# Kernel tuning notes

Measured on AMD Instinct MI355X. Metric: run time of the kernel, lower is better.

## Reference

```python
import jax, jax.numpy as jnp
import numpy as np
import math

B, S, HID = 2, 2048, 1024
NH = 16
HD = HID // NH


def setup_inputs() -> dict:
    key = jax.random.key(0)
    ks = jax.random.split(key, 5)
    std = 1.0 / math.sqrt(HID)
    return {
        "x": jax.random.normal(ks[0], (B, S, HID), dtype=jnp.float32),
        "wq": jax.random.normal(ks[1], (HID, HID), dtype=jnp.float32) * std,
        "wk": jax.random.normal(ks[2], (HID, HID), dtype=jnp.float32) * std,
        "wv": jax.random.normal(ks[3], (HID, HID), dtype=jnp.float32) * std,
        "wo": jax.random.normal(ks[4], (HID, HID), dtype=jnp.float32) * std,
    }


def reference(x, wq, wk, wv, wo):
    # x: [B, S, HID]; weights stored as nn.Linear weight [out, in] -> y = x @ W.T
    b, s, _ = x.shape
    scale = 1.0 / math.sqrt(HD)

    def heads(t):  # [B, S, HID] -> [B, NH, S, HD]
        return t.reshape(b, s, NH, HD).transpose(0, 2, 1, 3)

    q = heads(x @ wq.T)
    k = heads(x @ wk.T)
    v = heads(x @ wv.T)

    # single ring step (cp_size=1): streaming-LSE causal attention
    scores = jnp.einsum("bhqd,bhkd->bhqk", q, k) * scale  # [B, NH, S, S]
    q_idx = jnp.arange(s)[:, None]
    k_idx = jnp.arange(s)[None, :]
    causal_mask = k_idx > q_idx  # [S, S]
    scores = jnp.where(causal_mask, -jnp.inf, scores)

    local_max = jnp.max(scores, axis=-1, keepdims=True)
    exp_scores = jnp.exp(scores - local_max)
    local_sum = jnp.sum(exp_scores, axis=-1, keepdims=True)
    attn_num = jnp.einsum("bhqk,bhkd->bhqd", exp_scores, v)
    attn_out = attn_num / (local_sum + 1e-8)  # [B, NH, S, HD]

    attn_out = attn_out.transpose(0, 2, 1, 3).reshape(b, s, HID)
    return attn_out @ wo.T
```

## Files before the change

### kernel.cpp

```cpp
#include <hip/hip_runtime.h>
#include <hip/hip_bf16.h>

#define S_LEN 2048
#define NHEAD 16
#define HDIM 64
#define HID 1024
#define BATCH 2
#define TSTR 136

typedef __attribute__((ext_vector_type(8))) short s16x8;
typedef __attribute__((ext_vector_type(4))) short s16x4;
typedef __attribute__((ext_vector_type(4))) float f32x4;

__device__ __forceinline__ short f2bf(float f) {
    union { __hip_bfloat16 b; short s; } u;
    u.b = __float2bfloat16(f);
    return u.s;
}
__device__ __forceinline__ float fexp2(float x) {
    return __builtin_amdgcn_exp2f(x);
}
__device__ __forceinline__ f32x4 mfma16(s16x8 a, s16x8 b, f32x4 c) {
    return __builtin_amdgcn_mfma_f32_16x16x32_bf16(a, b, c, 0, 0, 0);
}
__device__ __forceinline__ void gload16(const short* g, short* l) {
    __builtin_amdgcn_global_load_lds(
        (const __attribute__((address_space(1))) void*)g,
        (__attribute__((address_space(3))) void*)l, 16, 0, 0);
}
__device__ __forceinline__ unsigned bfpack(float a, float b) {
    unsigned ua = __builtin_bit_cast(unsigned, a) + 0x8000u;
    unsigned ub = __builtin_bit_cast(unsigned, b) + 0x8000u;
    return (ub & 0xFFFF0000u) | (ua >> 16);
}

__global__ __launch_bounds__(256) void convert_kernel(
    const float* __restrict__ x,  const float* __restrict__ wq,
    const float* __restrict__ wk, const float* __restrict__ wv,
    const float* __restrict__ wo,
    short* __restrict__ xb, short* __restrict__ wcat, short* __restrict__ wob)
{
    const int F4X = 1048576, F4W = 262144;
    const int total = F4X + 4 * F4W;
    for (int i = blockIdx.x * blockDim.x + threadIdx.x; i < total;
         i += gridDim.x * blockDim.x) {
        const float4* s; short* d; int off;
        if (i < F4X)              { s = (const float4*)x;  d = xb;             off = i; }
        else if (i < F4X + F4W)   { s = (const float4*)wq; d = wcat;           off = i - F4X; }
        else if (i < F4X + 2*F4W) { s = (const float4*)wk; d = wcat + 1048576; off = i - (F4X + F4W); }
        else if (i < F4X + 3*F4W) { s = (const float4*)wv; d = wcat + 2097152; off = i - (F4X + 2*F4W); }
        else                      { s = (const float4*)wo; d = wob;            off = i - (F4X + 3*F4W); }
        float4 v = s[off];
        s16x4 o4 = { f2bf(v.x), f2bf(v.y), f2bf(v.z), f2bf(v.w) };
        *(s16x4*)(d + (size_t)off * 4) = o4;
    }
}

__global__ __launch_bounds__(256) void qkv_gemm2(
    const short* __restrict__ xb, const short* __restrict__ wcat,
    short* __restrict__ q_ws, short* __restrict__ k_ws, short* __restrict__ vt_ws)
{
    __shared__ union SM {
        struct { short A[128][64]; short B[128][64]; } s;
        short T[128][TSTR];
    } sm;
    const int t = threadIdx.x;
    const int lane = t & 63, w = t >> 6;
    const int g = lane >> 4, r15 = lane & 15;
    const int wm = w >> 1, wn = w & 1;
    const int bid = blockIdx.x;
    const int cx = bid & 7, ii = bid >> 3;
    const int mt = cx * 4 + (ii & 3), nt = ii >> 2;
    const int m0 = mt * 128, n0 = nt * 128;
    const int sel = n0 >> 10;
    const int nr0 = n0 & 1023;
    const short* Ag = (sel == 2) ? (wcat + (size_t)(2048 + nr0) * 1024)
                                 : (xb   + (size_t)m0 * 1024);
    const short* Bg = (sel == 2) ? (xb   + (size_t)m0 * 1024)
                                 : (wcat + (size_t)(sel * 1024 + nr0) * 1024);
    const int lrow = lane >> 3;
    const int scol = ((lane & 7) ^ lrow) * 8;
    const int rsw = r15 & 7;
    const float osc = (sel == 0) ? 0.125f : ((sel == 1) ? 1.44269504f : 1.0f);

    f32x4 acc[4][4] = {};

    for (int k0 = 0; k0 < 1024; k0 += 64) {
        __syncthreads();
        #pragma unroll
        for (int ch = 0; ch < 4; ++ch) {
            const int row = w * 32 + ch * 8;
            gload16(Ag + (size_t)(row + lrow) * 1024 + k0 + scol, &sm.s.A[row][0]);
            gload16(Bg + (size_t)(row + lrow) * 1024 + k0 + scol, &sm.s.B[row][0]);
        }
        __syncthreads();
        #pragma unroll
        for (int kk = 0; kk < 2; ++kk) {
            s16x8 af[4], bfr[4];
            #pragma unroll
            for (int mi = 0; mi < 4; ++mi)
                af[mi] = *(const s16x8*)&sm.s.A[wm * 64 + mi * 16 + r15][((kk * 4 + g) ^ rsw) * 8];
            #pragma unroll
            for (int ni = 0; ni < 4; ++ni)
                bfr[ni] = *(const s16x8*)&sm.s.B[wn * 64 + ni * 16 + r15][((kk * 4 + g) ^ rsw) * 8];
            #pragma unroll
            for (int mi = 0; mi < 4; ++mi)
                #pragma unroll
                for (int ni = 0; ni < 4; ++ni)
                    acc[mi][ni] = mfma16(af[mi], bfr[ni], acc[mi][ni]);
        }
    }

    __syncthreads();
    #pragma unroll
    for (int mi = 0; mi < 4; ++mi)
    #pragma unroll
    for (int ni = 0; ni < 4; ++ni)
        #pragma unroll
        for (int reg = 0; reg < 4; ++reg)
            sm.T[wm * 64 + mi * 16 + g * 4 + reg][wn * 64 + ni * 16 + r15]
                = f2bf(acc[mi][ni][reg] * osc);
    __syncthreads();

    const int b = m0 >> 11;
    const int ms = m0 & 2047;
    #pragma unroll
    for (int it = 0; it < 8; ++it) {
        int u = w + it * 4;
        int half = u & 1;
        int rg = u >> 1;
        int r = rg * 8 + lrow;
        int colc = half * 64 + (lane & 7) * 8;
        s16x8 v = *(const s16x8*)&sm.T[r][colc];
        if (sel == 2) {
            int n = nr0 + r;
            int h = n >> 6, d = n & 63;
            *(s16x8*)(vt_ws + ((size_t)(b * NHEAD + h) * HDIM + d) * S_LEN + ms + colc) = v;
        } else {
            int s = ms + r;
            int n = nr0 + colc;
            int h = n >> 6, d = n & 63;
            short* dst = (sel == 0) ? q_ws : k_ws;
            *(s16x8*)(dst + ((size_t)(b * NHEAD + h) * S_LEN + s) * HDIM + d) = v;
        }
    }
}

__global__ __launch_bounds__(128) void attn_kernel6(
    const short* __restrict__ q_ws, const short* __restrict__ k_ws,
    const short* __restrict__ vt_ws, short* __restrict__ attn_ws)
{
    __shared__ short Ks[2][64][64];
    __shared__ short Vts[2][64][64];
    const int t = threadIdx.x;
    const int lane = t & 63, w = t >> 6;
    const int g = lane >> 4, r15 = lane & 15;
    const int bid = blockIdx.x;
    const int lb = (bid & 7) * 128 + (bid >> 3);
    const int pi = lb & 31;
    const int bh = lb >> 5;
    const size_t base = (size_t)bh * S_LEN * HDIM;
    const int swr = (r15 & 7) << 3;
    const int b = bh >> 4, h = bh & 15;

    const int r0 = t >> 3, c0 = (t & 7) * 8;
    const int cx0 = c0 ^ ((r0 & 7) << 3);

    union P8 { unsigned u[4]; s16x8 v; };
    union V8 { s16x4 h[2]; s16x8 v; };

    for (int phase = 0; phase < 2; ++phase) {
        const int qt32 = phase ? (63 - pi) : pi;
        const int q0 = qt32 * 32;
        const int ntk = (qt32 >> 1) + 1;
        const int qg = q0 + w * 16 + r15;
        const int qrel = qg - (ntk - 1) * 64;
        s16x8 qf0 = *(const s16x8*)(q_ws + base + (size_t)qg * HDIM + g * 8);
        s16x8 qf1 = *(const s16x8*)(q_ws + base + (size_t)qg * HDIM + 32 + g * 8);
        f32x4 o[4] = {};
        float lrun_p = 0.f;

        #pragma unroll
        for (int j = 0; j < 4; ++j) {
            int r = r0 + j * 16;
            *(s16x8*)&Ks[0][r][cx0]  = *(const s16x8*)(k_ws  + base + (size_t)r * HDIM + c0);
            *(s16x8*)&Vts[0][r][cx0] = *(const s16x8*)(vt_ws + base + (size_t)r * S_LEN + c0);
        }
        __syncthreads();

        const short* kp = k_ws  + base + (size_t)(64 + r0) * HDIM + c0;
        const short* vp = vt_ws + base + (size_t)r0 * S_LEN + 64 + c0;

        for (int kt = 0; kt < ntk; ++kt) {
            const int cur = kt & 1;
            const bool pre = (kt + 1 < ntk);
            const bool dg = (kt == ntk - 1);
            s16x8 ka[4], va[4];
            if (pre) {
                #pragma unroll
                for (int j = 0; j < 4; ++j) {
                    ka[j] = *(const s16x8*)(kp + (size_t)j * 16 * HDIM);
                    va[j] = *(const s16x8*)(vp + (size_t)j * 16 * S_LEN);
                }
                kp += (size_t)64 * HDIM; vp += 64;
            }

            s16x8 kfa[4][2];
            #pragma unroll
            for (int f = 0; f < 4; ++f)
                #pragma unroll
                for (int c = 0; c < 2; ++c)
                    kfa[f][c] = *(const s16x8*)&Ks[cur][f * 16 + r15][(c * 32 + g * 8) ^ swr];
            V8 vfr[4][2];
            #pragma unroll
            for (int f2 = 0; f2 < 4; ++f2)
                #pragma unroll
                for (int kc = 0; kc < 2; ++kc) {
                    vfr[f2][kc].h[0] = *(const s16x4*)&Vts[cur][f2 * 16 + r15][(kc * 32 + g * 4) ^ swr];
                    vfr[f2][kc].h[1] = *(const s16x4*)&Vts[cur][f2 * 16 + r15][(kc * 32 + 16 + g * 4) ^ swr];
                }

            f32x4 z[4];
            __builtin_amdgcn_s_setprio(1);
            #pragma unroll
            for (int f = 0; f < 4; ++f) {
                f32x4 zz = { 0.f, 0.f, 0.f, 0.f };
                zz = mfma16(kfa[f][0], qf0, zz);
                zz = mfma16(kfa[f][1], qf1, zz);
                z[f] = zz;
            }
            __builtin_amdgcn_s_setprio(0);

            if (dg) {
                #pragma unroll
                for (int f = 0; f < 4; ++f)
                    #pragma unroll
                    for (int reg = 0; reg < 4; ++reg)
                        if (f * 16 + g * 4 + reg > qrel) z[f][reg] = -3e30f;
            }

            P8 p8[2];
            #pragma unroll
            for (int f = 0; f < 4; ++f) {
                float e0 = fexp2(z[f][0]);
                float e1 = fexp2(z[f][1]);
                float e2 = fexp2(z[f][2]);
                float e3 = fexp2(z[f][3]);
                lrun_p += (e0 + e1) + (e2 + e3);
                p8[f >> 1].u[(f & 1) * 2]     = bfpack(e0, e1);
                p8[f >> 1].u[(f & 1) * 2 + 1] = bfpack(e2, e3);
            }

            __builtin_amdgcn_s_setprio(1);
            #pragma unroll
            for (int f2 = 0; f2 < 4; ++f2) {
                o[f2] = mfma16(vfr[f2][0].v, p8[0].v, o[f2]);
                o[f2] = mfma16(vfr[f2][1].v, p8[1].v, o[f2]);
            }
            __builtin_amdgcn_s_setprio(0);

            if (pre) {
                #pragma unroll
                for (int j = 0; j < 4; ++j) {
                    int r = r0 + j * 16;
                    *(s16x8*)&Ks[cur ^ 1][r][cx0]  = ka[j];
                    *(s16x8*)&Vts[cur ^ 1][r][cx0] = va[j];
                }
            }
            __syncthreads();
        }

        float lr = lrun_p;
        lr += __shfl_xor(lr, 16);
        lr += __shfl_xor(lr, 32);
        float inv = 1.f / (lr + 1e-8f);
        size_t obase = ((size_t)b * S_LEN + qg) * HID + h * HDIM + g * 4;
        #pragma unroll
        for (int f2 = 0; f2 < 4; ++f2) {
            s16x4 ov = { f2bf(o[f2][0] * inv), f2bf(o[f2][1] * inv),
                         f2bf(o[f2][2] * inv), f2bf(o[f2][3] * inv) };
            *(s16x4*)(attn_ws + obase + f2 * 16) = ov;
        }
        __syncthreads();
    }
}

__global__ __launch_bounds__(256) void wo_gemm2(
    const short* __restrict__ attn, const short* __restrict__ wob,
    float* __restrict__ out)
{
    __shared__ short As[128][64];
    __shared__ short Bs[128][64];
    const int t = threadIdx.x;
    const int lane = t & 63, w = t >> 6;
    const int g = lane >> 4, r15 = lane & 15;
    const int wm = w >> 1, wn = w & 1;
    const int bid = blockIdx.x;
    const int cx = bid & 7, ii = bid >> 3;
    const int mt = cx * 4 + (ii & 3), nt = ii >> 2;
    const int m0 = mt * 128, n0 = nt * 128;
    const int lrow = lane >> 3;
    const int scol = ((lane & 7) ^ lrow) * 8;
    const int rsw = r15 & 7;

    f32x4 acc[4][4] = {};

    for (int k0 = 0; k0 < 1024; k0 += 64) {
        __syncthreads();
        #pragma unroll
        for (int ch = 0; ch < 4; ++ch) {
            const int row = w * 32 + ch * 8;
            gload16(attn + (size_t)(m0 + row + lrow) * 1024 + k0 + scol, &As[row][0]);
            gload16(wob  + (size_t)(n0 + row + lrow) * 1024 + k0 + scol, &Bs[row][0]);
        }
        __syncthreads();
        #pragma unroll
        for (int kk = 0; kk < 2; ++kk) {
            s16x8 af[4], bfr[4];
            #pragma unroll
            for (int mi = 0; mi < 4; ++mi)
                af[mi] = *(const s16x8*)&As[wm * 64 + mi * 16 + r15][((kk * 4 + g) ^ rsw) * 8];
            #pragma unroll
            for (int ni = 0; ni < 4; ++ni)
                bfr[ni] = *(const s16x8*)&Bs[wn * 64 + ni * 16 + r15][((kk * 4 + g) ^ rsw) * 8];
            #pragma unroll
            for (int mi = 0; mi < 4; ++mi)
                #pragma unroll
                for (int ni = 0; ni < 4; ++ni)
                    acc[mi][ni] = mfma16(af[mi], bfr[ni], acc[mi][ni]);
        }
    }

    #pragma unroll
    for (int mi = 0; mi < 4; ++mi)
    #pragma unroll
    for (int ni = 0; ni < 4; ++ni) {
        #pragma unroll
        for (int reg = 0; reg < 4; ++reg) {
            int m = m0 + wm * 64 + mi * 16 + g * 4 + reg;
            int n = n0 + wn * 64 + ni * 16 + r15;
            out[(size_t)m * 1024 + n] = acc[mi][ni][reg];
        }
    }
}

extern "C" void kernel_launch(void* const* d_in, const int* in_sizes, int n_in,
                              void* d_out, int out_size, void* d_ws, size_t ws_size,
                              hipStream_t stream) {
    const float* x  = (const float*)d_in[0];
    const float* wq = (const float*)d_in[1];
    const float* wk = (const float*)d_in[2];
    const float* wv = (const float*)d_in[3];
    const float* wo = (const float*)d_in[4];
    float* out = (float*)d_out;

    const size_t ELEMS = (size_t)BATCH * S_LEN * HID;
    short* q_ws    = (short*)d_ws;
    short* k_ws    = q_ws + ELEMS;
    short* vt_ws   = k_ws + ELEMS;
    short* xb      = vt_ws + ELEMS;
    short* attn_ws = xb;
    short* wcat    = xb + ELEMS;
    short* wob     = wcat + 3145728;

    convert_kernel<<<dim3(2048), dim3(256), 0, stream>>>(x, wq, wk, wv, wo, xb, wcat, wob);
    qkv_gemm2<<<dim3(768), dim3(256), 0, stream>>>(xb, wcat, q_ws, k_ws, vt_ws);
    attn_kernel6<<<dim3(1024), dim3(128), 0, stream>>>(q_ws, k_ws, vt_ws, attn_ws);
    wo_gemm2<<<dim3(256), dim3(256), 0, stream>>>(attn_ws, wob, out);
}
```

Baseline: 117.6 us.

## Process paired causal query tiles in one pass sharing K/V loads

```diff
diff --git a/kernel.cpp b/kernel.cpp
--- a/kernel.cpp
+++ b/kernel.cpp
@@ -146,7 +146,7 @@
     }
 }
 
-__global__ __launch_bounds__(128) void attn_kernel6(
+__global__ __launch_bounds__(128) void attn_kernel8(
     const short* __restrict__ q_ws, const short* __restrict__ k_ws,
     const short* __restrict__ vt_ws, short* __restrict__ attn_ws)
 {
@@ -156,9 +156,10 @@
     const int lane = t & 63, w = t >> 6;
     const int g = lane >> 4, r15 = lane & 15;
     const int bid = blockIdx.x;
-    const int lb = (bid & 7) * 128 + (bid >> 3);
-    const int pi = lb & 31;
-    const int bh = lb >> 5;
+    const int cx = bid & 7, ii = bid >> 3;
+    const int bh = cx * 4 + (ii >> 5);
+    const int v5 = ii & 31;
+    const int pi = (v5 & 1) ? (31 - (v5 >> 1)) : (v5 >> 1);
     const size_t base = (size_t)bh * S_LEN * HDIM;
     const int swr = (r15 & 7) << 3;
     const int b = bh >> 4, h = bh & 15;
@@ -169,76 +170,79 @@
     union P8 { unsigned u[4]; s16x8 v; };
     union V8 { s16x4 h[2]; s16x8 v; };
 
-    for (int phase = 0; phase < 2; ++phase) {
-        const int qt32 = phase ? (63 - pi) : pi;
-        const int q0 = qt32 * 32;
-        const int ntk = (qt32 >> 1) + 1;
-        const int qg = q0 + w * 16 + r15;
-        const int qrel = qg - (ntk - 1) * 64;
-        s16x8 qf0 = *(const s16x8*)(q_ws + base + (size_t)qg * HDIM + g * 8);
-        s16x8 qf1 = *(const s16x8*)(q_ws + base + (size_t)qg * HDIM + 32 + g * 8);
-        f32x4 o[4] = {};
-        float lrun_p = 0.f;
-
-        #pragma unroll
-        for (int j = 0; j < 4; ++j) {
-            int r = r0 + j * 16;
-            *(s16x8*)&Ks[0][r][cx0]  = *(const s16x8*)(k_ws  + base + (size_t)r * HDIM + c0);
-            *(s16x8*)&Vts[0][r][cx0] = *(const s16x8*)(vt_ws + base + (size_t)r * S_LEN + c0);
-        }
-        __syncthreads();
-
-        const short* kp = k_ws  + base + (size_t)(64 + r0) * HDIM + c0;
-        const short* vp = vt_ws + base + (size_t)r0 * S_LEN + 64 + c0;
-
-        for (int kt = 0; kt < ntk; ++kt) {
-            const int cur = kt & 1;
-            const bool pre = (kt + 1 < ntk);
-            const bool dg = (kt == ntk - 1);
-            s16x8 ka[4], va[4];
-            if (pre) {
-                #pragma unroll
-                for (int j = 0; j < 4; ++j) {
-                    ka[j] = *(const s16x8*)(kp + (size_t)j * 16 * HDIM);
-                    va[j] = *(const s16x8*)(vp + (size_t)j * 16 * S_LEN);
-                }
-                kp += (size_t)64 * HDIM; vp += 64;
-            }
-
-            s16x8 kfa[4][2];
-            #pragma unroll
-            for (int f = 0; f < 4; ++f)
-                #pragma unroll
-                for (int c = 0; c < 2; ++c)
-                    kfa[f][c] = *(const s16x8*)&Ks[cur][f * 16 + r15][(c * 32 + g * 8) ^ swr];
-            V8 vfr[4][2];
-            #pragma unroll
-            for (int f2 = 0; f2 < 4; ++f2)
-                #pragma unroll
-                for (int kc = 0; kc < 2; ++kc) {
-                    vfr[f2][kc].h[0] = *(const s16x4*)&Vts[cur][f2 * 16 + r15][(kc * 32 + g * 4) ^ swr];
-                    vfr[f2][kc].h[1] = *(const s16x4*)&Vts[cur][f2 * 16 + r15][(kc * 32 + 16 + g * 4) ^ swr];
-                }
-
+    const int qtA = pi, qtB = 63 - pi;
+    const int ntkA = (qtA >> 1) + 1;
+    const int ntkB = (qtB >> 1) + 1;
+    const int qgA = qtA * 32 + w * 16 + r15;
+    const int qgB = qtB * 32 + w * 16 + r15;
+    const int qrelA = qgA - (ntkA - 1) * 64;
+    const int qrelB = qgB - (ntkB - 1) * 64;
+
+    s16x8 qfA0 = *(const s16x8*)(q_ws + base + (size_t)qgA * HDIM + g * 8);
+    s16x8 qfA1 = *(const s16x8*)(q_ws + base + (size_t)qgA * HDIM + 32 + g * 8);
+    s16x8 qfB0 = *(const s16x8*)(q_ws + base + (size_t)qgB * HDIM + g * 8);
+    s16x8 qfB1 = *(const s16x8*)(q_ws + base + (size_t)qgB * HDIM + 32 + g * 8);
+    f32x4 oA[4] = {}, oB[4] = {};
+    float lrA = 0.f, lrB = 0.f;
+
+    #pragma unroll
+    for (int j = 0; j < 4; ++j) {
+        int r = r0 + j * 16;
+        *(s16x8*)&Ks[0][r][cx0]  = *(const s16x8*)(k_ws  + base + (size_t)r * HDIM + c0);
+        *(s16x8*)&Vts[0][r][cx0] = *(const s16x8*)(vt_ws + base + (size_t)r * S_LEN + c0);
+    }
+    __syncthreads();
+
+    const short* kp = k_ws  + base + (size_t)(64 + r0) * HDIM + c0;
+    const short* vp = vt_ws + base + (size_t)r0 * S_LEN + 64 + c0;
+
+    for (int kt = 0; kt < ntkB; ++kt) {
+        const int cur = kt & 1;
+        const bool pre = (kt + 1 < ntkB);
+        s16x8 ka[4], va[4];
+        if (pre) {
+            #pragma unroll
+            for (int j = 0; j < 4; ++j) {
+                ka[j] = *(const s16x8*)(kp + (size_t)j * 16 * HDIM);
+                va[j] = *(const s16x8*)(vp + (size_t)j * 16 * S_LEN);
+            }
+            kp += (size_t)64 * HDIM; vp += 64;
+        }
+
+        s16x8 kfa[4][2];
+        #pragma unroll
+        for (int f = 0; f < 4; ++f)
+            #pragma unroll
+            for (int c = 0; c < 2; ++c)
+                kfa[f][c] = *(const s16x8*)&Ks[cur][f * 16 + r15][(c * 32 + g * 8) ^ swr];
+        V8 vfr[4][2];
+        #pragma unroll
+        for (int f2 = 0; f2 < 4; ++f2)
+            #pragma unroll
+            for (int kc = 0; kc < 2; ++kc) {
+                vfr[f2][kc].h[0] = *(const s16x4*)&Vts[cur][f2 * 16 + r15][(kc * 32 + g * 4) ^ swr];
+                vfr[f2][kc].h[1] = *(const s16x4*)&Vts[cur][f2 * 16 + r15][(kc * 32 + 16 + g * 4) ^ swr];
+            }
+
+        {
+            const bool dg = (kt == ntkB - 1);
             f32x4 z[4];
             __builtin_amdgcn_s_setprio(1);
             #pragma unroll
             for (int f = 0; f < 4; ++f) {
                 f32x4 zz = { 0.f, 0.f, 0.f, 0.f };
-                zz = mfma16(kfa[f][0], qf0, zz);
-                zz = mfma16(kfa[f][1], qf1, zz);
+                zz = mfma16(kfa[f][0], qfB0, zz);
+                zz = mfma16(kfa[f][1], qfB1, zz);
                 z[f] = zz;
             }
             __builtin_amdgcn_s_setprio(0);
-
             if (dg) {
                 #pragma unroll
                 for (int f = 0; f < 4; ++f)
                     #pragma unroll
                     for (int reg = 0; reg < 4; ++reg)
-                        if (f * 16 + g * 4 + reg > qrel) z[f][reg] = -3e30f;
-            }
-
+                        if (f * 16 + g * 4 + reg > qrelB) z[f][reg] = -3e30f;
+            }
             P8 p8[2];
             #pragma unroll
             for (int f = 0; f < 4; ++f) {
@@ -246,42 +250,94 @@
                 float e1 = fexp2(z[f][1]);
                 float e2 = fexp2(z[f][2]);
                 float e3 = fexp2(z[f][3]);
-                lrun_p += (e0 + e1) + (e2 + e3);
+                lrB += (e0 + e1) + (e2 + e3);
                 p8[f >> 1].u[(f & 1) * 2]     = bfpack(e0, e1);
                 p8[f >> 1].u[(f & 1) * 2 + 1] = bfpack(e2, e3);
             }
-
             __builtin_amdgcn_s_setprio(1);
             #pragma unroll
             for (int f2 = 0; f2 < 4; ++f2) {
-                o[f2] = mfma16(vfr[f2][0].v, p8[0].v, o[f2]);
-                o[f2] = mfma16(vfr[f2][1].v, p8[1].v, o[f2]);
+                oB[f2] = mfma16(vfr[f2][0].v, p8[0].v, oB[f2]);
+                oB[f2] = mfma16(vfr[f2][1].v, p8[1].v, oB[f2]);
             }
             __builtin_amdgcn_s_setprio(0);
-
-            if (pre) {
+        }
+
+        if (kt < ntkA) {
+            const bool dg = (kt == ntkA - 1);
+            f32x4 z[4];
+            __builtin_amdgcn_s_setprio(1);
+            #pragma unroll
+            for (int f = 0; f < 4; ++f) {
+                f32x4 zz = { 0.f, 0.f, 0.f, 0.f };
+                zz = mfma16(kfa[f][0], qfA0, zz);
+                zz = mfma16(kfa[f][1], qfA1, zz);
+                z[f] = zz;
+            }
+            __builtin_amdgcn_s_setprio(0);
+            if (dg) {
                 #pragma unroll
-                for (int j = 0; j < 4; ++j) {
-                    int r = r0 + j * 16;
-                    *(s16x8*)&Ks[cur ^ 1][r][cx0]  = ka[j];
-                    *(s16x8*)&Vts[cur ^ 1][r][cx0] = va[j];
-                }
-            }
-            __syncthreads();
-        }
-
-        float lr = lrun_p;
-        lr += __shfl_xor(lr, 16);
-        lr += __shfl_xor(lr, 32);
-        float inv = 1.f / (lr + 1e-8f);
-        size_t obase = ((size_t)b * S_LEN + qg) * HID + h * HDIM + g * 4;
+                for (int f = 0; f < 4; ++f)
+                    #pragma unroll
+                    for (int reg = 0; reg < 4; ++reg)
+                        if (f * 16 + g * 4 + reg > qrelA) z[f][reg] = -3e30f;
+            }
+            P8 p8[2];
+            #pragma unroll
+            for (int f = 0; f < 4; ++f) {
+                float e0 = fexp2(z[f][0]);
+                float e1 = fexp2(z[f][1]);
+                float e2 = fexp2(z[f][2]);
+                float e3 = fexp2(z[f][3]);
+                lrA += (e0 + e1) + (e2 + e3);
+                p8[f >> 1].u[(f & 1) * 2]     = bfpack(e0, e1);
+                p8[f >> 1].u[(f & 1) * 2 + 1] = bfpack(e2, e3);
+            }
+            __builtin_amdgcn_s_setprio(1);
+            #pragma unroll
+            for (int f2 = 0; f2 < 4; ++f2) {
+                oA[f2] = mfma16(vfr[f2][0].v, p8[0].v, oA[f2]);
+                oA[f2] = mfma16(vfr[f2][1].v, p8[1].v, oA[f2]);
+            }
+            __builtin_amdgcn_s_setprio(0);
+        }
+
+        if (pre) {
+            #pragma unroll
+            for (int j = 0; j < 4; ++j) {
+                int r = r0 + j * 16;
+                *(s16x8*)&Ks[cur ^ 1][r][cx0]  = ka[j];
+                *(s16x8*)&Vts[cur ^ 1][r][cx0] = va[j];
+            }
+        }
+        __syncthreads();
+    }
+
+    {
+        float l = lrA;
+        l += __shfl_xor(l, 16);
+        l += __shfl_xor(l, 32);
+        float inv = 1.f / (l + 1e-8f);
+        size_t obase = ((size_t)b * S_LEN + qgA) * HID + h * HDIM + g * 4;
         #pragma unroll
         for (int f2 = 0; f2 < 4; ++f2) {
-            s16x4 ov = { f2bf(o[f2][0] * inv), f2bf(o[f2][1] * inv),
-                         f2bf(o[f2][2] * inv), f2bf(o[f2][3] * inv) };
+            s16x4 ov = { f2bf(oA[f2][0] * inv), f2bf(oA[f2][1] * inv),
+                         f2bf(oA[f2][2] * inv), f2bf(oA[f2][3] * inv) };
             *(s16x4*)(attn_ws + obase + f2 * 16) = ov;
         }
-        __syncthreads();
+    }
+    {
+        float l = lrB;
+        l += __shfl_xor(l, 16);
+        l += __shfl_xor(l, 32);
+        float inv = 1.f / (l + 1e-8f);
+        size_t obase = ((size_t)b * S_LEN + qgB) * HID + h * HDIM + g * 4;
+        #pragma unroll
+        for (int f2 = 0; f2 < 4; ++f2) {
+            s16x4 ov = { f2bf(oB[f2][0] * inv), f2bf(oB[f2][1] * inv),
+                         f2bf(oB[f2][2] * inv), f2bf(oB[f2][3] * inv) };
+            *(s16x4*)(attn_ws + obase + f2 * 16) = ov;
+        }
     }
 }
 
@@ -365,6 +421,6 @@
 
     convert_kernel<<<dim3(2048), dim3(256), 0, stream>>>(x, wq, wk, wv, wo, xb, wcat, wob);
     qkv_gemm2<<<dim3(768), dim3(256), 0, stream>>>(xb, wcat, q_ws, k_ws, vt_ws);
-    attn_kernel6<<<dim3(1024), dim3(128), 0, stream>>>(q_ws, k_ws, vt_ws, attn_ws);
+    attn_kernel8<<<dim3(1024), dim3(128), 0, stream>>>(q_ws, k_ws, vt_ws, attn_ws);
     wo_gemm2<<<dim3(256), dim3(256), 0, stream>>>(attn_ws, wob, out);
 }
```

Measured after the change: 120.6 us. 1.03x slower.

## Enlarge attention query tile to 64 rows per block to reuse K/V tiles

Applied to the files above, without the earlier changes.

```diff
diff --git a/kernel.cpp b/kernel.cpp
--- a/kernel.cpp
+++ b/kernel.cpp
@@ -146,7 +146,7 @@
     }
 }
 
-__global__ __launch_bounds__(128) void attn_kernel6(
+__global__ __launch_bounds__(128) void attn_kernel9(
     const short* __restrict__ q_ws, const short* __restrict__ k_ws,
     const short* __restrict__ vt_ws, short* __restrict__ attn_ws)
 {
@@ -156,9 +156,9 @@
     const int lane = t & 63, w = t >> 6;
     const int g = lane >> 4, r15 = lane & 15;
     const int bid = blockIdx.x;
-    const int lb = (bid & 7) * 128 + (bid >> 3);
-    const int pi = lb & 31;
-    const int bh = lb >> 5;
+    const int lb = (bid & 7) * 64 + (bid >> 3);
+    const int pi = lb & 15;
+    const int bh = lb >> 4;
     const size_t base = (size_t)bh * S_LEN * HDIM;
     const int swr = (r15 & 7) << 3;
     const int b = bh >> 4, h = bh & 15;
@@ -170,15 +170,19 @@
     union V8 { s16x4 h[2]; s16x8 v; };
 
     for (int phase = 0; phase < 2; ++phase) {
-        const int qt32 = phase ? (63 - pi) : pi;
-        const int q0 = qt32 * 32;
-        const int ntk = (qt32 >> 1) + 1;
-        const int qg = q0 + w * 16 + r15;
-        const int qrel = qg - (ntk - 1) * 64;
-        s16x8 qf0 = *(const s16x8*)(q_ws + base + (size_t)qg * HDIM + g * 8);
-        s16x8 qf1 = *(const s16x8*)(q_ws + base + (size_t)qg * HDIM + 32 + g * 8);
-        f32x4 o[4] = {};
-        float lrun_p = 0.f;
+        const int qt = phase ? (31 - pi) : pi;
+        const int q0 = qt * 64;
+        const int ntk = qt + 1;
+
+        s16x8 qf[2][2];
+        #pragma unroll
+        for (int m = 0; m < 2; ++m)
+            #pragma unroll
+            for (int c = 0; c < 2; ++c)
+                qf[m][c] = *(const s16x8*)(q_ws + base +
+                    (size_t)(q0 + w * 32 + m * 16 + r15) * HDIM + c * 32 + g * 8);
+        f32x4 o[2][4] = {};
+        float lr[2] = { 0.f, 0.f };
 
         #pragma unroll
         for (int j = 0; j < 4; ++j) {
@@ -220,44 +224,48 @@
                     vfr[f2][kc].h[1] = *(const s16x4*)&Vts[cur][f2 * 16 + r15][(kc * 32 + 16 + g * 4) ^ swr];
                 }
 
-            f32x4 z[4];
-            __builtin_amdgcn_s_setprio(1);
-            #pragma unroll
-            for (int f = 0; f < 4; ++f) {
-                f32x4 zz = { 0.f, 0.f, 0.f, 0.f };
-                zz = mfma16(kfa[f][0], qf0, zz);
-                zz = mfma16(kfa[f][1], qf1, zz);
-                z[f] = zz;
+            #pragma unroll
+            for (int m = 0; m < 2; ++m) {
+                f32x4 z[4];
+                __builtin_amdgcn_s_setprio(1);
+                #pragma unroll
+                for (int f = 0; f < 4; ++f) {
+                    f32x4 zz = { 0.f, 0.f, 0.f, 0.f };
+                    zz = mfma16(kfa[f][0], qf[m][0], zz);
+                    zz = mfma16(kfa[f][1], qf[m][1], zz);
+                    z[f] = zz;
+                }
+                __builtin_amdgcn_s_setprio(0);
+
+                if (dg) {
+                    const int qrel = w * 32 + m * 16 + r15;
+                    #pragma unroll
+                    for (int f = 0; f < 4; ++f)
+                        #pragma unroll
+                        for (int reg = 0; reg < 4; ++reg)
+                            if (f * 16 + g * 4 + reg > qrel) z[f][reg] = -3e30f;
+                }
+
+                P8 p8[2];
+                #pragma unroll
+                for (int f = 0; f < 4; ++f) {
+                    float e0 = fexp2(z[f][0]);
+                    float e1 = fexp2(z[f][1]);
+                    float e2 = fexp2(z[f][2]);
+                    float e3 = fexp2(z[f][3]);
+                    lr[m] += (e0 + e1) + (e2 + e3);
+                    p8[f >> 1].u[(f & 1) * 2]     = bfpack(e0, e1);
+                    p8[f >> 1].u[(f & 1) * 2 + 1] = bfpack(e2, e3);
+                }
+
+                __builtin_amdgcn_s_setprio(1);
+                #pragma unroll
+                for (int f2 = 0; f2 < 4; ++f2) {
+                    o[m][f2] = mfma16(vfr[f2][0].v, p8[0].v, o[m][f2]);
+                    o[m][f2] = mfma16(vfr[f2][1].v, p8[1].v, o[m][f2]);
+                }
+                __builtin_amdgcn_s_setprio(0);
             }
-            __builtin_amdgcn_s_setprio(0);
-
-            if (dg) {
-                #pragma unroll
-                for (int f = 0; f < 4; ++f)
-                    #pragma unroll
-                    for (int reg = 0; reg < 4; ++reg)
-                        if (f * 16 + g * 4 + reg > qrel) z[f][reg] = -3e30f;
-            }
-
-            P8 p8[2];
-            #pragma unroll
-            for (int f = 0; f < 4; ++f) {
-                float e0 = fexp2(z[f][0]);
-                float e1 = fexp2(z[f][1]);
-                float e2 = fexp2(z[f][2]);
-                float e3 = fexp2(z[f][3]);
-                lrun_p += (e0 + e1) + (e2 + e3);
-                p8[f >> 1].u[(f & 1) * 2]     = bfpack(e0, e1);
-                p8[f >> 1].u[(f & 1) * 2 + 1] = bfpack(e2, e3);
-            }
-
-            __builtin_amdgcn_s_setprio(1);
-            #pragma unroll
-            for (int f2 = 0; f2 < 4; ++f2) {
-                o[f2] = mfma16(vfr[f2][0].v, p8[0].v, o[f2]);
-                o[f2] = mfma16(vfr[f2][1].v, p8[1].v, o[f2]);
-            }
-            __builtin_amdgcn_s_setprio(0);
 
             if (pre) {
                 #pragma unroll
@@ -270,16 +278,20 @@
             __syncthreads();
         }
 
-        float lr = lrun_p;
-        lr += __shfl_xor(lr, 16);
-        lr += __shfl_xor(lr, 32);
-        float inv = 1.f / (lr + 1e-8f);
-        size_t obase = ((size_t)b * S_LEN + qg) * HID + h * HDIM + g * 4;
-        #pragma unroll
-        for (int f2 = 0; f2 < 4; ++f2) {
-            s16x4 ov = { f2bf(o[f2][0] * inv), f2bf(o[f2][1] * inv),
-                         f2bf(o[f2][2] * inv), f2bf(o[f2][3] * inv) };
-            *(s16x4*)(attn_ws + obase + f2 * 16) = ov;
+        #pragma unroll
+        for (int m = 0; m < 2; ++m) {
+            float l = lr[m];
+            l += __shfl_xor(l, 16);
+            l += __shfl_xor(l, 32);
+            float inv = 1.f / (l + 1e-8f);
+            const int qg = q0 + w * 32 + m * 16 + r15;
+            size_t obase = ((size_t)b * S_LEN + qg) * HID + h * HDIM + g * 4;
+            #pragma unroll
+            for (int f2 = 0; f2 < 4; ++f2) {
+                s16x4 ov = { f2bf(o[m][f2][0] * inv), f2bf(o[m][f2][1] * inv),
+                             f2bf(o[m][f2][2] * inv), f2bf(o[m][f2][3] * inv) };
+                *(s16x4*)(attn_ws + obase + f2 * 16) = ov;
+            }
         }
         __syncthreads();
     }
@@ -365,6 +377,6 @@
 
     convert_kernel<<<dim3(2048), dim3(256), 0, stream>>>(x, wq, wk, wv, wo, xb, wcat, wob);
     qkv_gemm2<<<dim3(768), dim3(256), 0, stream>>>(xb, wcat, q_ws, k_ws, vt_ws);
-    attn_kernel6<<<dim3(1024), dim3(128), 0, stream>>>(q_ws, k_ws, vt_ws, attn_ws);
+    attn_kernel9<<<dim3(512), dim3(128), 0, stream>>>(q_ws, k_ws, vt_ws, attn_ws);
     wo_gemm2<<<dim3(256), dim3(256), 0, stream>>>(attn_ws, wob, out);
 }
```

Result: no change. 116.2 us (-1.1%).
